# Performance work log

Hardware: AMD Instinct MI355X
Metric: run time of the kernel (lower is better)

## Reference

```python
import jax, jax.numpy as jnp
import numpy as np

N_NODES = 100000
N_EDGES = 1600000
VOCAB = 2048
NODE_DIM = 64
HIDDEN = 64
N_MASK = 10000


def setup_inputs() -> dict:
    key = jax.random.key(0)
    ks = jax.random.split(key, 10)
    x = jax.random.randint(ks[0], (N_NODES, 1), 0, VOCAB, dtype=jnp.int64)
    edge_index = jax.random.randint(ks[1], (2, N_EDGES), 0, N_NODES, dtype=jnp.int64)
    mask_x_position = jax.random.randint(ks[2], (N_MASK,), 0, N_NODES, dtype=jnp.int64)
    # embedding init: normal with std = node_dim ** -0.5 (as in initialize_parameters)
    emb = jax.random.normal(ks[3], (VOCAB, NODE_DIM), dtype=jnp.float32) * (NODE_DIM ** -0.5)
    # SAGEConv layer 1: lin_l (neighbors, with bias), lin_r (root, no bias)
    s1 = (NODE_DIM ** -0.5)
    W_l1 = jax.random.uniform(ks[4], (NODE_DIM, HIDDEN), jnp.float32, -s1, s1)
    b_l1 = jnp.zeros((HIDDEN,), jnp.float32)
    W_r1 = jax.random.uniform(ks[5], (NODE_DIM, HIDDEN), jnp.float32, -s1, s1)
    # SAGEConv layer 2
    s2 = (HIDDEN ** -0.5)
    W_l2 = jax.random.uniform(ks[6], (HIDDEN, VOCAB), jnp.float32, -s2, s2)
    b_l2 = jnp.zeros((VOCAB,), jnp.float32)
    W_r2 = jax.random.uniform(ks[7], (HIDDEN, VOCAB), jnp.float32, -s2, s2)
    return {"x": x, "edge_index": edge_index, "mask_x_position": mask_x_position,
            "emb": emb, "W_l1": W_l1, "b_l1": b_l1, "W_r1": W_r1,
            "W_l2": W_l2, "b_l2": b_l2, "W_r2": W_r2}


def _sage_conv(h, src, dst, W_l, b_l, W_r):
    # mean-aggregate source-node features at destination nodes (PyG SAGEConv, aggr='mean')
    msgs = h[src]                                                  # [E, D]
    agg = jax.ops.segment_sum(msgs, dst, num_segments=N_NODES)     # [N, D]
    deg = jax.ops.segment_sum(jnp.ones((src.shape[0], 1), h.dtype), dst,
                              num_segments=N_NODES)                # [N, 1]
    mean = agg / jnp.maximum(deg, 1.0)
    return mean @ W_l + b_l + h @ W_r


def reference(x, edge_index, mask_x_position, emb, W_l1, b_l1, W_r1, W_l2, b_l2, W_r2):
    src, dst = edge_index[0], edge_index[1]
    h = emb[x[:, 0]]                                # embedding(x).squeeze(1) -> [N, node_dim]
    # dropout is identity in eval mode
    h = _sage_conv(h, src, dst, W_l1, b_l1, W_r1)   # [N, hidden]
    h = jax.nn.relu(h)
    h = _sage_conv(h, src, dst, W_l2, b_l2, W_r2)   # [N, vocab]
    return jax.nn.log_softmax(h[mask_x_position], axis=1)
```

## Files before the change

kernel.cpp:

```cpp
#include <hip/hip_runtime.h>
#include <math.h>

#define N_NODES   100000
#define N_EDGES   1600000
#define VOCAB     2048
#define NODE_DIM  64
#define HIDDEN    64
#define N_MASK    10000

#define BN        192
#define NBKT      521
#define CHUNK     4096
#define NCH       391

typedef __attribute__((ext_vector_type(8))) short short8;
typedef __attribute__((ext_vector_type(4))) float f32x4;
typedef unsigned short ushort_t;
typedef unsigned int uint_t;

#define H1_OFF      0
#define ESRC_OFF    25600000
#define EVOC_OFF    32000000
#define E2_OFF      38400000
#define EWL_OFF     38400000
#define EWR_OFF     38924288
#define W2T_OFF     39448576
#define X2B_OFF     39972864
#define ROWPTR_OFF  51200000
#define BCNT_OFF    51600016
#define BPTR_OFF    51602112
#define BCUR_OFF    51604208

__device__ __forceinline__ ushort_t f2bf(float f) {
    uint_t u = __builtin_bit_cast(uint_t, f);
    u += 0x7FFFu + ((u >> 16) & 1u);
    return (ushort_t)(u >> 16);
}

__global__ __launch_bounds__(256) void k_prep(const float* __restrict__ emb,
                                              const float* __restrict__ Wl1,
                                              const float* __restrict__ Wr1,
                                              const float* __restrict__ Wl2,
                                              const float* __restrict__ Wr2,
                                              float* __restrict__ embWl,
                                              float* __restrict__ embWr,
                                              ushort_t* __restrict__ W2T) {
    __shared__ ushort_t T[64 * 66];
    const int bx = blockIdx.x;
    const int tid = threadIdx.x;
    if (bx < 1024) {
        const int half = bx >> 9;
        const float* W = half ? Wr1 : Wl1;
        float* out = half ? embWr : embWl;
        int idx = (bx & 511) * 256 + tid;
        int v = idx >> 6, c = idx & 63;
        float s = 0.0f;
#pragma unroll 8
        for (int k = 0; k < 64; k++) s += emb[v * 64 + k] * W[k * 64 + c];
        out[idx] = s;
    } else {
        int t = bx - 1024;
        const int k0 = (t & 1) * 64;
        const int n0 = (t >> 1) * 64;
        const float* Wsrc = (k0 == 0) ? Wl2 : Wr2;
#pragma unroll
        for (int i = 0; i < 16; i++) {
            int idx = i * 256 + tid;
            int k = idx >> 6, n = idx & 63;
            T[n * 66 + k] = f2bf(Wsrc[(size_t)k * VOCAB + n0 + n]);
        }
        __syncthreads();
#pragma unroll
        for (int i = 0; i < 16; i++) {
            int idx = i * 256 + tid;
            int n = idx >> 6, k = idx & 63;
            W2T[(size_t)(n0 + n) * 128 + k0 + k] = T[n * 66 + k];
        }
    }
}

__global__ __launch_bounds__(256) void k_count(const int* __restrict__ dst,
                                               int* __restrict__ bcnt) {
    __shared__ int hist[NBKT];
    for (int i = threadIdx.x; i < NBKT; i += 256) hist[i] = 0;
    __syncthreads();
    int stride = gridDim.x * 256;
    for (int e = blockIdx.x * 256 + threadIdx.x; e < N_EDGES; e += stride)
        atomicAdd(&hist[dst[e] / BN], 1);
    __syncthreads();
    for (int i = threadIdx.x; i < NBKT; i += 256) {
        int c = hist[i];
        if (c) atomicAdd(&bcnt[i], c);
    }
}

__global__ __launch_bounds__(1024) void k_bscan(const int* __restrict__ bcnt,
                                                int* __restrict__ bptr,
                                                int* __restrict__ bcur,
                                                int* __restrict__ rowptr) {
    __shared__ int s[1024];
    int t = threadIdx.x;
    int v = (t < NBKT) ? bcnt[t] : 0;
    s[t] = v;
    __syncthreads();
    for (int off = 1; off < 1024; off <<= 1) {
        int a = (t >= off) ? s[t - off] : 0;
        __syncthreads();
        s[t] += a;
        __syncthreads();
    }
    if (t < NBKT) { bptr[t] = s[t] - v; bcur[t] = s[t] - v; }
    if (t == NBKT - 1) bptr[NBKT] = s[t];
    if (t == 0) rowptr[N_NODES] = N_EDGES;
}

__global__ __launch_bounds__(256) void k_scatter2(const int* __restrict__ src,
                                                  const int* __restrict__ dst,
                                                  const int* __restrict__ x,
                                                  int* __restrict__ bcur,
                                                  int2* __restrict__ e2) {
    __shared__ uint_t dstb[CHUNK];
    __shared__ int hist[NBKT];
    const int e0 = blockIdx.x * CHUNK;
    const int n = min(CHUNK, N_EDGES - e0);
    for (int i = threadIdx.x; i < NBKT; i += 256) hist[i] = 0;
    __syncthreads();
    for (int i = threadIdx.x; i < n; i += 256) {
        int d = dst[e0 + i];
        int b = d / BN;
        dstb[i] = ((uint_t)b << 8) | (uint_t)(d - b * BN);
        atomicAdd(&hist[b], 1);
    }
    __syncthreads();
    for (int i = threadIdx.x; i < NBKT; i += 256) {
        int c = hist[i];
        hist[i] = c ? atomicAdd(&bcur[i], c) : 0;
    }
    __syncthreads();
    for (int i = threadIdx.x; i < n; i += 256) {
        uint_t db = dstb[i];
        int b = db >> 8;
        int s = src[e0 + i];
        int voc = x[s];
        int pos = atomicAdd(&hist[b], 1);
        e2[pos] = make_int2(s, (voc << 8) | (int)(db & 255u));
    }
}

__global__ __launch_bounds__(256) void k_sortb(const int* __restrict__ bptr,
                                               const int2* __restrict__ e2,
                                               int* __restrict__ rowptr,
                                               int* __restrict__ esrc,
                                               int* __restrict__ evoc) {
    __shared__ int cnt[BN];
    __shared__ int s[256];
    __shared__ int cur[BN];
    const int b = blockIdx.x;
    const int t = threadIdx.x;
    const int r0 = bptr[b], r1 = bptr[b + 1];
    if (t < BN) cnt[t] = 0;
    __syncthreads();
    for (int e = r0 + t; e < r1; e += 256)
        atomicAdd(&cnt[e2[e].y & 255], 1);
    __syncthreads();
    int v = (t < BN) ? cnt[t] : 0;
    s[t] = v;
    __syncthreads();
    for (int off = 1; off < 256; off <<= 1) {
        int a = (t >= off) ? s[t - off] : 0;
        __syncthreads();
        s[t] += a;
        __syncthreads();
    }
    if (t < BN) {
        int excl = s[t] - v;
        cur[t] = excl;
        int node = b * BN + t;
        if (node < N_NODES) rowptr[node] = r0 + excl;
    }
    __syncthreads();
    for (int e = r0 + t; e < r1; e += 256) {
        int2 ev = e2[e];
        int pos = r0 + atomicAdd(&cur[ev.y & 255], 1);
        esrc[pos] = ev.x;
        evoc[pos] = ev.y >> 8;
    }
}

__global__ __launch_bounds__(256) void k_agg1(const int* __restrict__ rowptr,
                                              const int* __restrict__ evoc,
                                              const int* __restrict__ x,
                                              const float* __restrict__ embWl,
                                              const float* __restrict__ embWr,
                                              const float* __restrict__ b1,
                                              float* __restrict__ h1) {
    int gw = (blockIdx.x * 256 + threadIdx.x) >> 6;
    int lane = threadIdx.x & 63;
    if (gw >= N_NODES) return;
    int r0 = rowptr[gw], r1 = rowptr[gw + 1];
    int deg = r1 - r0;
    float s0 = 0.0f, s1 = 0.0f, s2 = 0.0f, s3 = 0.0f;
    for (int base = 0; base < deg; base += 64) {
        int cnt = min(64, deg - base);
        int myv = (base + lane < deg) ? evoc[r0 + base + lane] : 0;
        int t = 0;
        for (; t + 3 < cnt; t += 4) {
            int va = __shfl(myv, t);
            int vb = __shfl(myv, t + 1);
            int vc = __shfl(myv, t + 2);
            int vd = __shfl(myv, t + 3);
            s0 += embWl[(va << 6) + lane];
            s1 += embWl[(vb << 6) + lane];
            s2 += embWl[(vc << 6) + lane];
            s3 += embWl[(vd << 6) + lane];
        }
        for (; t < cnt; t++)
            s0 += embWl[(__shfl(myv, t) << 6) + lane];
    }
    float sum = (s0 + s1) + (s2 + s3);
    float inv = 1.0f / fmaxf((float)deg, 1.0f);
    float self = embWr[(x[gw] << 6) + lane];
    h1[((size_t)gw << 6) + lane] = fmaxf(sum * inv + self + b1[lane], 0.0f);
}

__global__ __launch_bounds__(256) void k_x2(const int* __restrict__ mask,
                                            const int* __restrict__ rowptr,
                                            const int* __restrict__ esrc,
                                            const float* __restrict__ h1,
                                            ushort_t* __restrict__ X2b) {
    int gw = (blockIdx.x * 256 + threadIdx.x) >> 6;
    int lane = threadIdx.x & 63;
    if (gw >= N_MASK) return;
    int n = mask[gw];
    int r0 = rowptr[n], r1 = rowptr[n + 1];
    int deg = r1 - r0;
    float s0 = 0.0f, s1 = 0.0f, s2 = 0.0f, s3 = 0.0f;
    for (int base = 0; base < deg; base += 64) {
        int cnt = min(64, deg - base);
        int mys = (base + lane < deg) ? esrc[r0 + base + lane] : 0;
        int t = 0;
        for (; t + 3 < cnt; t += 4) {
            int sa = __shfl(mys, t);
            int sb = __shfl(mys, t + 1);
            int sc = __shfl(mys, t + 2);
            int sd = __shfl(mys, t + 3);
            s0 += h1[((size_t)sa << 6) + lane];
            s1 += h1[((size_t)sb << 6) + lane];
            s2 += h1[((size_t)sc << 6) + lane];
            s3 += h1[((size_t)sd << 6) + lane];
        }
        for (; t < cnt; t++)
            s0 += h1[((size_t)__shfl(mys, t) << 6) + lane];
    }
    float sum = (s0 + s1) + (s2 + s3);
    float inv = 1.0f / fmaxf((float)deg, 1.0f);
    X2b[gw * 128 + lane]      = f2bf(sum * inv);
    X2b[gw * 128 + 64 + lane] = f2bf(h1[((size_t)n << 6) + lane]);
}

__global__ __launch_bounds__(256) void k_gemm2_mfma(const ushort_t* __restrict__ X2b,
                                                    const ushort_t* __restrict__ W2T,
                                                    const float* __restrict__ bias,
                                                    float* __restrict__ out,
                                                    int M) {
    __shared__ ushort_t As[64 * 144];
    __shared__ ushort_t Bs[64 * 144];
    const int tid  = threadIdx.x;
    const int row0 = blockIdx.x * 64;
    const int col0 = blockIdx.y * 64;

#pragma unroll
    for (int i = 0; i < 4; i++) {
        int idx = i * 256 + tid;
        int r = idx >> 4, ch = idx & 15;
        int R = row0 + r;
        short8 v = {0, 0, 0, 0, 0, 0, 0, 0};
        if (R < M) v = *(const short8*)(X2b + (size_t)R * 128 + ch * 8);
        *(short8*)(As + r * 144 + ch * 8) = v;
    }
#pragma unroll
    for (int i = 0; i < 4; i++) {
        int idx = i * 256 + tid;
        int r = idx >> 4, ch = idx & 15;
        *(short8*)(Bs + r * 144 + ch * 8) =
            *(const short8*)(W2T + (size_t)(col0 + r) * 128 + ch * 8);
    }
    __syncthreads();

    const int lane = tid & 63;
    const int wv   = tid >> 6;
    const int wr = wv >> 1, wc = wv & 1;
    const int l15 = lane & 15, q = lane >> 4;

    f32x4 acc[2][2] = {};
    const ushort_t* Abase = As + (wr * 32 + l15) * 144 + q * 8;
    const ushort_t* Bbase = Bs + (wc * 32 + l15) * 144 + q * 8;

#pragma unroll
    for (int ks = 0; ks < 4; ks++) {
        short8 a0 = *(const short8*)(Abase + ks * 32);
        short8 a1 = *(const short8*)(Abase + 16 * 144 + ks * 32);
        short8 b0 = *(const short8*)(Bbase + ks * 32);
        short8 b1 = *(const short8*)(Bbase + 16 * 144 + ks * 32);
        acc[0][0] = __builtin_amdgcn_mfma_f32_16x16x32_bf16(a0, b0, acc[0][0], 0, 0, 0);
        acc[0][1] = __builtin_amdgcn_mfma_f32_16x16x32_bf16(a0, b1, acc[0][1], 0, 0, 0);
        acc[1][0] = __builtin_amdgcn_mfma_f32_16x16x32_bf16(a1, b0, acc[1][0], 0, 0, 0);
        acc[1][1] = __builtin_amdgcn_mfma_f32_16x16x32_bf16(a1, b1, acc[1][1], 0, 0, 0);
    }

#pragma unroll
    for (int ni = 0; ni < 2; ni++) {
        int c_ = col0 + wc * 32 + ni * 16 + l15;
        float bv = bias[c_];
#pragma unroll
        for (int mi = 0; mi < 2; mi++) {
#pragma unroll
            for (int reg = 0; reg < 4; reg++) {
                int r_ = row0 + wr * 32 + mi * 16 + q * 4 + reg;
                if (r_ < M) out[(size_t)r_ * VOCAB + c_] = acc[mi][ni][reg] + bv;
            }
        }
    }
}

__global__ __launch_bounds__(256) void k_logsoftmax(float* __restrict__ out) {
    const int row = blockIdx.x;
    float4* p4 = (float4*)(out + (size_t)row * VOCAB);
    const int tid = threadIdx.x;
    float4 v[2];
    float m = -INFINITY;
#pragma unroll
    for (int i = 0; i < 2; i++) {
        v[i] = p4[tid + i * 256];
        m = fmaxf(m, fmaxf(fmaxf(v[i].x, v[i].y), fmaxf(v[i].z, v[i].w)));
    }
#pragma unroll
    for (int off = 1; off < 64; off <<= 1) m = fmaxf(m, __shfl_xor(m, off));
    __shared__ float redm[4];
    __shared__ float reds[4];
    int wave = tid >> 6;
    if ((tid & 63) == 0) redm[wave] = m;
    __syncthreads();
    m = fmaxf(fmaxf(redm[0], redm[1]), fmaxf(redm[2], redm[3]));
    float s = 0.0f;
#pragma unroll
    for (int i = 0; i < 2; i++)
        s += expf(v[i].x - m) + expf(v[i].y - m) + expf(v[i].z - m) + expf(v[i].w - m);
#pragma unroll
    for (int off = 1; off < 64; off <<= 1) s += __shfl_xor(s, off);
    if ((tid & 63) == 0) reds[wave] = s;
    __syncthreads();
    s = reds[0] + reds[1] + reds[2] + reds[3];
    float L = m + logf(s);
#pragma unroll
    for (int i = 0; i < 2; i++) {
        float4 o = v[i];
        o.x -= L; o.y -= L; o.z -= L; o.w -= L;
        p4[tid + i * 256] = o;
    }
}

extern "C" void kernel_launch(void* const* d_in, const int* in_sizes, int n_in,
                              void* d_out, int out_size, void* d_ws, size_t ws_size,
                              hipStream_t stream) {
    const int*   x    = (const int*)d_in[0];
    const int*   ei   = (const int*)d_in[1];
    const int*   src  = ei;
    const int*   dst  = ei + N_EDGES;
    const int*   mask = (const int*)d_in[2];
    const float* emb  = (const float*)d_in[3];
    const float* Wl1  = (const float*)d_in[4];
    const float* bl1  = (const float*)d_in[5];
    const float* Wr1  = (const float*)d_in[6];
    const float* Wl2  = (const float*)d_in[7];
    const float* bl2  = (const float*)d_in[8];
    const float* Wr2  = (const float*)d_in[9];
    float* out = (float*)d_out;

    char* ws = (char*)d_ws;
    float*    h1     = (float*)(ws + H1_OFF);
    int*      esrc   = (int*)(ws + ESRC_OFF);
    int*      evoc   = (int*)(ws + EVOC_OFF);
    int2*     e2     = (int2*)(ws + E2_OFF);
    float*    embWl  = (float*)(ws + EWL_OFF);
    float*    embWr  = (float*)(ws + EWR_OFF);
    ushort_t* W2T    = (ushort_t*)(ws + W2T_OFF);
    ushort_t* X2b    = (ushort_t*)(ws + X2B_OFF);
    int*      rowptr = (int*)(ws + ROWPTR_OFF);
    int*      bcnt   = (int*)(ws + BCNT_OFF);
    int*      bptr   = (int*)(ws + BPTR_OFF);
    int*      bcur   = (int*)(ws + BCUR_OFF);

    hipMemsetAsync(ws + BCNT_OFF, 0, 2096, stream);

    k_count   <<<512, 256, 0, stream>>>(dst, bcnt);
    k_bscan   <<<1, 1024, 0, stream>>>(bcnt, bptr, bcur, rowptr);
    k_scatter2<<<NCH, 256, 0, stream>>>(src, dst, x, bcur, e2);
    k_sortb   <<<NBKT, 256, 0, stream>>>(bptr, e2, rowptr, esrc, evoc);

    k_prep<<<1088, 256, 0, stream>>>(emb, Wl1, Wr1, Wl2, Wr2, embWl, embWr, W2T);

    k_agg1<<<(N_NODES * 64 + 255) / 256, 256, 0, stream>>>(rowptr, evoc, x, embWl, embWr, bl1, h1);

    k_x2<<<(N_MASK * 64 + 255) / 256, 256, 0, stream>>>(mask, rowptr, esrc, h1, X2b);
    dim3 g2((N_MASK + 63) / 64, VOCAB / 64);
    k_gemm2_mfma<<<g2, 256, 0, stream>>>(X2b, W2T, bl2, out, N_MASK);

    k_logsoftmax<<<N_MASK, 256, 0, stream>>>(out);
}
```

Baseline: 295.1 us.

## Fuse GEMM2 with log-softmax and precompute per-chunk scatter offsets

Two independent changes. First, the bucket-sort counting pass now writes a per-chunk, per-bucket histogram matrix, and a new column-scan kernel turns it into exact write offsets. The scatter kernel then places edges with only shared-memory atomics, with no second local histogram and no global atomic reservation. Second, the output GEMM and log-softmax are fused: each block computes 16 full rows of 2048 logits in registers via MFMA, reduces max and sum across waves, and writes the final log-probabilities once, avoiding a write and re-read of the 80MB logits buffer. This adds a kernel launch, 128 accumulator registers per thread (lower occupancy), W2T re-read per block from cache, and fast __expf/__logf.

```diff
diff --git a/kernel.cpp b/kernel.cpp
--- a/kernel.cpp
+++ b/kernel.cpp
@@ -10,8 +10,8 @@
 
 #define BN        192
 #define NBKT      521
-#define CHUNK     4096
-#define NCH       391
+#define CHUNK     2048
+#define NCH       782
 
 typedef __attribute__((ext_vector_type(8))) short short8;
 typedef __attribute__((ext_vector_type(4))) float f32x4;
@@ -29,7 +29,7 @@
 #define ROWPTR_OFF  51200000
 #define BCNT_OFF    51600016
 #define BPTR_OFF    51602112
-#define BCUR_OFF    51604208
+#define HMAT_OFF    51604224
 
 __device__ __forceinline__ ushort_t f2bf(float f) {
     uint_t u = __builtin_bit_cast(uint_t, f);
@@ -79,24 +79,26 @@
     }
 }
 
-__global__ __launch_bounds__(256) void k_count(const int* __restrict__ dst,
-                                               int* __restrict__ bcnt) {
+__global__ __launch_bounds__(256) void k_hist2d(const int* __restrict__ dst,
+                                                int* __restrict__ H,
+                                                int* __restrict__ bcnt) {
     __shared__ int hist[NBKT];
     for (int i = threadIdx.x; i < NBKT; i += 256) hist[i] = 0;
     __syncthreads();
-    int stride = gridDim.x * 256;
-    for (int e = blockIdx.x * 256 + threadIdx.x; e < N_EDGES; e += stride)
-        atomicAdd(&hist[dst[e] / BN], 1);
+    const int e0 = blockIdx.x * CHUNK;
+    const int n = min(CHUNK, N_EDGES - e0);
+    for (int i = threadIdx.x; i < n; i += 256)
+        atomicAdd(&hist[dst[e0 + i] / BN], 1);
     __syncthreads();
     for (int i = threadIdx.x; i < NBKT; i += 256) {
         int c = hist[i];
+        H[blockIdx.x * NBKT + i] = c;
         if (c) atomicAdd(&bcnt[i], c);
     }
 }
 
 __global__ __launch_bounds__(1024) void k_bscan(const int* __restrict__ bcnt,
                                                 int* __restrict__ bptr,
-                                                int* __restrict__ bcur,
                                                 int* __restrict__ rowptr) {
     __shared__ int s[1024];
     int t = threadIdx.x;
@@ -109,41 +111,48 @@
         s[t] += a;
         __syncthreads();
     }
-    if (t < NBKT) { bptr[t] = s[t] - v; bcur[t] = s[t] - v; }
+    if (t < NBKT) bptr[t] = s[t] - v;
     if (t == NBKT - 1) bptr[NBKT] = s[t];
     if (t == 0) rowptr[N_NODES] = N_EDGES;
+}
+
+__global__ __launch_bounds__(64) void k_cscan(const int* __restrict__ bptr,
+                                              int* __restrict__ H) {
+    const int k = blockIdx.x;
+    const int lane = threadIdx.x;
+    int run = bptr[k];
+    for (int base = 0; base < NCH; base += 64) {
+        int c = base + lane;
+        int v = (c < NCH) ? H[c * NBKT + k] : 0;
+        int incl = v;
+#pragma unroll
+        for (int off = 1; off < 64; off <<= 1) {
+            int t = __shfl_up(incl, off);
+            if (lane >= off) incl += t;
+        }
+        if (c < NCH) H[c * NBKT + k] = run + incl - v;
+        run += __shfl(incl, 63);
+    }
 }
 
 __global__ __launch_bounds__(256) void k_scatter2(const int* __restrict__ src,
                                                   const int* __restrict__ dst,
                                                   const int* __restrict__ x,
-                                                  int* __restrict__ bcur,
+                                                  const int* __restrict__ H,
                                                   int2* __restrict__ e2) {
-    __shared__ uint_t dstb[CHUNK];
-    __shared__ int hist[NBKT];
+    __shared__ int cur[NBKT];
+    for (int i = threadIdx.x; i < NBKT; i += 256)
+        cur[i] = H[blockIdx.x * NBKT + i];
+    __syncthreads();
     const int e0 = blockIdx.x * CHUNK;
     const int n = min(CHUNK, N_EDGES - e0);
-    for (int i = threadIdx.x; i < NBKT; i += 256) hist[i] = 0;
-    __syncthreads();
     for (int i = threadIdx.x; i < n; i += 256) {
         int d = dst[e0 + i];
         int b = d / BN;
-        dstb[i] = ((uint_t)b << 8) | (uint_t)(d - b * BN);
-        atomicAdd(&hist[b], 1);
-    }
-    __syncthreads();
-    for (int i = threadIdx.x; i < NBKT; i += 256) {
-        int c = hist[i];
-        hist[i] = c ? atomicAdd(&bcur[i], c) : 0;
-    }
-    __syncthreads();
-    for (int i = threadIdx.x; i < n; i += 256) {
-        uint_t db = dstb[i];
-        int b = db >> 8;
         int s = src[e0 + i];
         int voc = x[s];
-        int pos = atomicAdd(&hist[b], 1);
-        e2[pos] = make_int2(s, (voc << 8) | (int)(db & 255u));
+        int pos = atomicAdd(&cur[b], 1);
+        e2[pos] = make_int2(s, (voc << 8) | (d - b * BN));
     }
 }
 
@@ -258,105 +267,82 @@
     X2b[gw * 128 + 64 + lane] = f2bf(h1[((size_t)n << 6) + lane]);
 }
 
-__global__ __launch_bounds__(256) void k_gemm2_mfma(const ushort_t* __restrict__ X2b,
-                                                    const ushort_t* __restrict__ W2T,
-                                                    const float* __restrict__ bias,
-                                                    float* __restrict__ out,
-                                                    int M) {
-    __shared__ ushort_t As[64 * 144];
-    __shared__ ushort_t Bs[64 * 144];
+__global__ __launch_bounds__(256) void k_gemm2ls(const ushort_t* __restrict__ X2b,
+                                                 const ushort_t* __restrict__ W2T,
+                                                 const float* __restrict__ bias,
+                                                 float* __restrict__ out) {
     const int tid  = threadIdx.x;
-    const int row0 = blockIdx.x * 64;
-    const int col0 = blockIdx.y * 64;
-
-#pragma unroll
-    for (int i = 0; i < 4; i++) {
-        int idx = i * 256 + tid;
-        int r = idx >> 4, ch = idx & 15;
-        int R = row0 + r;
-        short8 v = {0, 0, 0, 0, 0, 0, 0, 0};
-        if (R < M) v = *(const short8*)(X2b + (size_t)R * 128 + ch * 8);
-        *(short8*)(As + r * 144 + ch * 8) = v;
-    }
-#pragma unroll
-    for (int i = 0; i < 4; i++) {
-        int idx = i * 256 + tid;
-        int r = idx >> 4, ch = idx & 15;
-        *(short8*)(Bs + r * 144 + ch * 8) =
-            *(const short8*)(W2T + (size_t)(col0 + r) * 128 + ch * 8);
-    }
-    __syncthreads();
-
     const int lane = tid & 63;
-    const int wv   = tid >> 6;
-    const int wr = wv >> 1, wc = wv & 1;
-    const int l15 = lane & 15, q = lane >> 4;
-
-    f32x4 acc[2][2] = {};
-    const ushort_t* Abase = As + (wr * 32 + l15) * 144 + q * 8;
-    const ushort_t* Bbase = Bs + (wc * 32 + l15) * 144 + q * 8;
-
-#pragma unroll
-    for (int ks = 0; ks < 4; ks++) {
-        short8 a0 = *(const short8*)(Abase + ks * 32);
-        short8 a1 = *(const short8*)(Abase + 16 * 144 + ks * 32);
-        short8 b0 = *(const short8*)(Bbase + ks * 32);
-        short8 b1 = *(const short8*)(Bbase + 16 * 144 + ks * 32);
-        acc[0][0] = __builtin_amdgcn_mfma_f32_16x16x32_bf16(a0, b0, acc[0][0], 0, 0, 0);
-        acc[0][1] = __builtin_amdgcn_mfma_f32_16x16x32_bf16(a0, b1, acc[0][1], 0, 0, 0);
-        acc[1][0] = __builtin_amdgcn_mfma_f32_16x16x32_bf16(a1, b0, acc[1][0], 0, 0, 0);
-        acc[1][1] = __builtin_amdgcn_mfma_f32_16x16x32_bf16(a1, b1, acc[1][1], 0, 0, 0);
-    }
-
-#pragma unroll
-    for (int ni = 0; ni < 2; ni++) {
-        int c_ = col0 + wc * 32 + ni * 16 + l15;
-        float bv = bias[c_];
-#pragma unroll
-        for (int mi = 0; mi < 2; mi++) {
-#pragma unroll
-            for (int reg = 0; reg < 4; reg++) {
-                int r_ = row0 + wr * 32 + mi * 16 + q * 4 + reg;
-                if (r_ < M) out[(size_t)r_ * VOCAB + c_] = acc[mi][ni][reg] + bv;
-            }
-        }
-    }
-}
-
-__global__ __launch_bounds__(256) void k_logsoftmax(float* __restrict__ out) {
-    const int row = blockIdx.x;
-    float4* p4 = (float4*)(out + (size_t)row * VOCAB);
-    const int tid = threadIdx.x;
-    float4 v[2];
-    float m = -INFINITY;
-#pragma unroll
-    for (int i = 0; i < 2; i++) {
-        v[i] = p4[tid + i * 256];
-        m = fmaxf(m, fmaxf(fmaxf(v[i].x, v[i].y), fmaxf(v[i].z, v[i].w)));
-    }
-#pragma unroll
-    for (int off = 1; off < 64; off <<= 1) m = fmaxf(m, __shfl_xor(m, off));
-    __shared__ float redm[4];
-    __shared__ float reds[4];
-    int wave = tid >> 6;
-    if ((tid & 63) == 0) redm[wave] = m;
-    __syncthreads();
-    m = fmaxf(fmaxf(redm[0], redm[1]), fmaxf(redm[2], redm[3]));
-    float s = 0.0f;
-#pragma unroll
-    for (int i = 0; i < 2; i++)
-        s += expf(v[i].x - m) + expf(v[i].y - m) + expf(v[i].z - m) + expf(v[i].w - m);
-#pragma unroll
-    for (int off = 1; off < 64; off <<= 1) s += __shfl_xor(s, off);
-    if ((tid & 63) == 0) reds[wave] = s;
-    __syncthreads();
-    s = reds[0] + reds[1] + reds[2] + reds[3];
-    float L = m + logf(s);
-#pragma unroll
-    for (int i = 0; i < 2; i++) {
-        float4 o = v[i];
-        o.x -= L; o.y -= L; o.z -= L; o.w -= L;
-        p4[tid + i * 256] = o;
+    const int w    = tid >> 6;
+    const int l15  = lane & 15, q = lane >> 4;
+    const int row0 = blockIdx.x * 16;
+
+    const ushort_t* Arow = X2b + (size_t)(row0 + l15) * 128 + q * 8;
+    short8 a[4];
+#pragma unroll
+    for (int ks = 0; ks < 4; ks++) a[ks] = *(const short8*)(Arow + ks * 32);
+
+    f32x4 acc[32];
+#pragma unroll
+    for (int c = 0; c < 32; c++) {
+        const int colbase = c * 64 + w * 16;
+        float bv = bias[colbase + l15];
+        acc[c] = (f32x4){bv, bv, bv, bv};
+        const ushort_t* Brow = W2T + (size_t)(colbase + l15) * 128 + q * 8;
+#pragma unroll
+        for (int ks = 0; ks < 4; ks++) {
+            short8 b = *(const short8*)(Brow + ks * 32);
+            acc[c] = __builtin_amdgcn_mfma_f32_16x16x32_bf16(a[ks], b, acc[c], 0, 0, 0);
+        }
+    }
+
+    float rmax[4] = {-INFINITY, -INFINITY, -INFINITY, -INFINITY};
+#pragma unroll
+    for (int c = 0; c < 32; c++)
+#pragma unroll
+        for (int r = 0; r < 4; r++) rmax[r] = fmaxf(rmax[r], acc[c][r]);
+#pragma unroll
+    for (int off = 1; off < 16; off <<= 1)
+#pragma unroll
+        for (int r = 0; r < 4; r++) rmax[r] = fmaxf(rmax[r], __shfl_xor(rmax[r], off));
+    __shared__ float smax[4][16];
+    __shared__ float ssum[4][16];
+    if (l15 == 0)
+#pragma unroll
+        for (int r = 0; r < 4; r++) smax[w][q * 4 + r] = rmax[r];
+    __syncthreads();
+#pragma unroll
+    for (int r = 0; r < 4; r++) {
+        int row = q * 4 + r;
+        rmax[r] = fmaxf(fmaxf(smax[0][row], smax[1][row]),
+                        fmaxf(smax[2][row], smax[3][row]));
+    }
+    float rsum[4] = {0.0f, 0.0f, 0.0f, 0.0f};
+#pragma unroll
+    for (int c = 0; c < 32; c++)
+#pragma unroll
+        for (int r = 0; r < 4; r++) rsum[r] += __expf(acc[c][r] - rmax[r]);
+#pragma unroll
+    for (int off = 1; off < 16; off <<= 1)
+#pragma unroll
+        for (int r = 0; r < 4; r++) rsum[r] += __shfl_xor(rsum[r], off);
+    if (l15 == 0)
+#pragma unroll
+        for (int r = 0; r < 4; r++) ssum[w][q * 4 + r] = rsum[r];
+    __syncthreads();
+    float L[4];
+#pragma unroll
+    for (int r = 0; r < 4; r++) {
+        int row = q * 4 + r;
+        L[r] = rmax[r] + __logf(ssum[0][row] + ssum[1][row] +
+                                ssum[2][row] + ssum[3][row]);
+    }
+#pragma unroll
+    for (int c = 0; c < 32; c++) {
+        int col = c * 64 + w * 16 + l15;
+#pragma unroll
+        for (int r = 0; r < 4; r++)
+            out[(size_t)(row0 + q * 4 + r) * VOCAB + col] = acc[c][r] - L[r];
     }
 }
 
@@ -389,13 +375,14 @@
     int*      rowptr = (int*)(ws + ROWPTR_OFF);
     int*      bcnt   = (int*)(ws + BCNT_OFF);
     int*      bptr   = (int*)(ws + BPTR_OFF);
-    int*      bcur   = (int*)(ws + BCUR_OFF);
+    int*      Hm     = (int*)(ws + HMAT_OFF);
 
     hipMemsetAsync(ws + BCNT_OFF, 0, 2096, stream);
 
-    k_count   <<<512, 256, 0, stream>>>(dst, bcnt);
-    k_bscan   <<<1, 1024, 0, stream>>>(bcnt, bptr, bcur, rowptr);
-    k_scatter2<<<NCH, 256, 0, stream>>>(src, dst, x, bcur, e2);
+    k_hist2d  <<<NCH, 256, 0, stream>>>(dst, Hm, bcnt);
+    k_bscan   <<<1, 1024, 0, stream>>>(bcnt, bptr, rowptr);
+    k_cscan   <<<NBKT, 64, 0, stream>>>(bptr, Hm);
+    k_scatter2<<<NCH, 256, 0, stream>>>(src, dst, x, Hm, e2);
     k_sortb   <<<NBKT, 256, 0, stream>>>(bptr, e2, rowptr, esrc, evoc);
 
     k_prep<<<1088, 256, 0, stream>>>(emb, Wl1, Wr1, Wl2, Wr2, embWl, embWr, W2T);
@@ -403,8 +390,5 @@
     k_agg1<<<(N_NODES * 64 + 255) / 256, 256, 0, stream>>>(rowptr, evoc, x, embWl, embWr, bl1, h1);
 
     k_x2<<<(N_MASK * 64 + 255) / 256, 256, 0, stream>>>(mask, rowptr, esrc, h1, X2b);
-    dim3 g2((N_MASK + 63) / 64, VOCAB / 64);
-    k_gemm2_mfma<<<g2, 256, 0, stream>>>(X2b, W2T, bl2, out, N_MASK);
-
-    k_logsoftmax<<<N_MASK, 256, 0, stream>>>(out);
-}
+    k_gemm2ls<<<N_MASK / 16, 256, 0, stream>>>(X2b, W2T, bl2, out);
+}
```

Measured after the change: 309.2 us. +4.8%, slower.
